# Optimization experiments

Measured on AMD Instinct MI355X. Metric: run time of the kernel, lower is better.

Reference implementation:

```python
import jax, jax.numpy as jnp
import numpy as np

L, B, S, D, H, FF, V = 4, 2, 1024, 768, 12, 3072, 50257
HD = D // H  # 64
EPS = 1e-5


def _ln(x, w, b):
    m = jnp.mean(x, axis=-1, keepdims=True)
    v = jnp.mean(jnp.square(x - m), axis=-1, keepdims=True)
    return (x - m) * jax.lax.rsqrt(v + EPS) * w + b


def setup_inputs() -> dict:
    key = jax.random.key(0)
    ks = jax.random.split(key, 8)
    std = 0.02
    inp = {
        'input_ids': jax.random.randint(ks[0], (B, S), 0, V),
        'tok_emb': jax.random.normal(ks[1], (V, D), jnp.float32) * std,
        'pos_emb': jax.random.normal(ks[2], (S, D), jnp.float32) * std,
        'ln1_w': jnp.ones((L, D), jnp.float32),
        'ln1_b': jnp.zeros((L, D), jnp.float32),
        'qkv_w': jax.random.normal(ks[3], (L, 3 * D, D), jnp.float32) * std,
        'qkv_b': jnp.zeros((L, 3 * D), jnp.float32),
        'out_w': jax.random.normal(ks[4], (L, D, D), jnp.float32) * std,
        'out_b': jnp.zeros((L, D), jnp.float32),
        'ln2_w': jnp.ones((L, D), jnp.float32),
        'ln2_b': jnp.zeros((L, D), jnp.float32),
        'fc1_w': jax.random.normal(ks[5], (L, FF, D), jnp.float32) * std,
        'fc1_b': jnp.zeros((L, FF), jnp.float32),
        'fc2_w': jax.random.normal(ks[6], (L, D, FF), jnp.float32) * std,
        'fc2_b': jnp.zeros((L, D), jnp.float32),
        'lnf_w': jnp.ones((D,), jnp.float32),
        'lnf_b': jnp.zeros((D,), jnp.float32),
    }
    return inp


def _gpt_forward(input_ids, tok_emb, pos_emb, ln1_w, ln1_b, qkv_w, qkv_b,
                 out_w, out_b, ln2_w, ln2_b, fc1_w, fc1_b, fc2_w, fc2_b,
                 lnf_w, lnf_b):
    x = tok_emb[input_ids] + pos_emb[None, :S, :]  # [B,S,D]
    causal = jnp.tril(jnp.ones((S, S), bool))  # [S,S]
    scale = 1.0 / np.sqrt(HD)
    for l in range(L):
        # --- attention ---
        h = _ln(x, ln1_w[l], ln1_b[l])
        qkv = h @ qkv_w[l].T + qkv_b[l]  # [B,S,3D]
        qkv = qkv.reshape(B, S, 3, H, HD).transpose(2, 0, 3, 1, 4)
        q, k, v = qkv[0], qkv[1], qkv[2]  # [B,H,S,HD]
        scores = jnp.einsum('bhqd,bhkd->bhqk', q, k) * scale
        scores = jnp.where(causal, scores, -jnp.inf)
        w = jax.nn.softmax(scores, axis=-1)
        a = jnp.einsum('bhqk,bhkd->bhqd', w, v)  # [B,H,S,HD]
        a = a.transpose(0, 2, 1, 3).reshape(B, S, D)
        x = x + a @ out_w[l].T + out_b[l]
        # --- ffn ---
        h = _ln(x, ln2_w[l], ln2_b[l])
        h = jax.nn.gelu(h @ fc1_w[l].T + fc1_b[l], approximate=False)
        x = x + h @ fc2_w[l].T + fc2_b[l]
    x = _ln(x, lnf_w, lnf_b)
    logits = x @ tok_emb.T  # tied lm_head, no bias
    return logits


def reference(input_ids, tok_emb, pos_emb, ln1_w, ln1_b, qkv_w, qkv_b,
              out_w, out_b, ln2_w, ln2_b, fc1_w, fc1_b, fc2_w, fc2_b,
              lnf_w, lnf_b):
    return _gpt_forward(input_ids, tok_emb, pos_emb, ln1_w, ln1_b, qkv_w,
                        qkv_b, out_w, out_b, ln2_w, ln2_b, fc1_w, fc1_b,
                        fc2_w, fc2_b, lnf_w, lnf_b)
```

## Files before the change

### kernel.cpp

```cpp
#include <hip/hip_runtime.h>
#include <cstdint>
#include <cstddef>

#define D_MODEL 768
#define NHEAD   12
#define SEQ     1024
#define NTOK    2048
#define FFDIM   3072
#define NLAYER  4
#define VOCAB   50257
#define QKVD    2304

typedef float f32x4 __attribute__((ext_vector_type(4)));
typedef __bf16 bf16x8 __attribute__((ext_vector_type(8)));

__device__ __forceinline__ unsigned short f2bf(float f) {
  unsigned int u = __float_as_uint(f);
  return (unsigned short)((u + 0x7FFFu + ((u >> 16) & 1u)) >> 16);
}

__global__ __launch_bounds__(256) void k_cvt(const float* __restrict__ in,
                                             unsigned short* __restrict__ out, int n8) {
  int i = blockIdx.x * 256 + threadIdx.x;
  if (i >= n8) return;
  const float4* p = (const float4*)in;
  float4 a = p[2 * i], b = p[2 * i + 1];
  union { unsigned short u[8]; uint4 v; } r;
  r.u[0] = f2bf(a.x); r.u[1] = f2bf(a.y); r.u[2] = f2bf(a.z); r.u[3] = f2bf(a.w);
  r.u[4] = f2bf(b.x); r.u[5] = f2bf(b.y); r.u[6] = f2bf(b.z); r.u[7] = f2bf(b.w);
  ((uint4*)out)[i] = r.v;
}

__global__ __launch_bounds__(256) void k_embed(const int* __restrict__ ids,
                                               const float* __restrict__ tok,
                                               const float* __restrict__ pos,
                                               float* __restrict__ x) {
  int gid = blockIdx.x * 256 + threadIdx.x;
  int t = gid / 192, f = gid - t * 192;
  int id = ids[t];
  float4 a = ((const float4*)tok)[(size_t)id * 192 + f];
  float4 b = ((const float4*)pos)[(size_t)(t & (SEQ - 1)) * 192 + f];
  float4 o; o.x = a.x + b.x; o.y = a.y + b.y; o.z = a.z + b.z; o.w = a.w + b.w;
  ((float4*)x)[gid] = o;
}

__global__ __launch_bounds__(256) void k_ln(const float* __restrict__ x,
                                            const float* __restrict__ w,
                                            const float* __restrict__ b,
                                            unsigned short* __restrict__ out) {
  __shared__ float red[256];
  int row = blockIdx.x, tid = threadIdx.x;
  const float* xr = x + (size_t)row * D_MODEL;
  float v0 = xr[tid], v1 = xr[tid + 256], v2 = xr[tid + 512];
  red[tid] = v0 + v1 + v2;
  __syncthreads();
  for (int o = 128; o > 0; o >>= 1) { if (tid < o) red[tid] += red[tid + o]; __syncthreads(); }
  float mean = red[0] * (1.0f / 768.0f);
  __syncthreads();
  float d0 = v0 - mean, d1 = v1 - mean, d2 = v2 - mean;
  red[tid] = d0 * d0 + d1 * d1 + d2 * d2;
  __syncthreads();
  for (int o = 128; o > 0; o >>= 1) { if (tid < o) red[tid] += red[tid + o]; __syncthreads(); }
  float rstd = rsqrtf(red[0] * (1.0f / 768.0f) + 1e-5f);
  unsigned short* orow = out + (size_t)row * D_MODEL;
  orow[tid]       = f2bf(d0 * rstd * w[tid]       + b[tid]);
  orow[tid + 256] = f2bf(d1 * rstd * w[tid + 256] + b[tid + 256]);
  orow[tid + 512] = f2bf(d2 * rstd * w[tid + 512] + b[tid + 512]);
}

__global__ __launch_bounds__(256) void k_vt(const unsigned short* __restrict__ qkv,
                                            unsigned short* __restrict__ vt) {
  __shared__ unsigned short t[64][80];
  int bid = blockIdx.x;
  int st = bid & 15, h = (bid >> 4) % NHEAD, b = bid / (16 * NHEAD);
  int tid = threadIdx.x;
  int r = tid >> 2, cq = (tid & 3) * 16;
  const unsigned short* src =
      qkv + (size_t)(b * SEQ + st * 64 + r) * QKVD + 2 * D_MODEL + h * 64 + cq;
  *(uint4*)&t[r][cq] = *(const uint4*)src;
  *(uint4*)&t[r][cq + 8] = *(const uint4*)(src + 8);
  __syncthreads();
  int d = r, j0 = cq;
  unsigned short* dst = vt + ((size_t)(b * D_MODEL) + h * 64 + d) * SEQ + st * 64 + j0;
  union { unsigned short u[8]; uint4 v; } o0, o1;
  #pragma unroll
  for (int jj = 0; jj < 8; ++jj) o0.u[jj] = t[j0 + jj][d];
  #pragma unroll
  for (int jj = 0; jj < 8; ++jj) o1.u[jj] = t[j0 + 8 + jj][d];
  *(uint4*)dst = o0.v;
  *(uint4*)(dst + 8) = o1.v;
}

__global__ __launch_bounds__(64) void k_attn(const unsigned short* __restrict__ qkv,
                                             const unsigned short* __restrict__ vt,
                                             unsigned short* __restrict__ attO) {
  int bid = blockIdx.x;
  int qt = (SEQ / 16 - 1) - (bid & 63);
  int h = (bid >> 6) % NHEAD;
  int b = bid / (64 * NHEAD);
  int lane = threadIdx.x;
  int fr = lane & 15, fq = lane >> 4;
  int qb = qt * 16;

  size_t rowQ = (size_t)(b * SEQ + qb + fr) * QKVD + h * 64;
  bf16x8 bq0 = *(const bf16x8*)(qkv + rowQ + fq * 8);
  bf16x8 bq1 = *(const bf16x8*)(qkv + rowQ + 32 + fq * 8);

  float m = -1e30f, ll = 0.0f;
  f32x4 o[4] = {};
  int nkt = (qt >> 1) + 1;
  size_t kvrow0 = (size_t)(b * SEQ) * QKVD;
  const unsigned short* vbase0 = vt + ((size_t)(b * D_MODEL) + h * 64 + fr) * SEQ;

  for (int kt = 0; kt < nkt; ++kt) {
    int kvb = kt * 32;
    bool diag = (kt == nkt - 1);
    float p[2][4];
    float tm = -1e30f;
    #pragma unroll
    for (int t = 0; t < 2; ++t) {
      size_t rowK = kvrow0 + (size_t)(kvb + t * 16 + fr) * QKVD + D_MODEL + h * 64;
      bf16x8 ak0 = *(const bf16x8*)(qkv + rowK + fq * 8);
      bf16x8 ak1 = *(const bf16x8*)(qkv + rowK + 32 + fq * 8);
      f32x4 st = {};
      st = __builtin_amdgcn_mfma_f32_16x16x32_bf16(ak0, bq0, st, 0, 0, 0);
      st = __builtin_amdgcn_mfma_f32_16x16x32_bf16(ak1, bq1, st, 0, 0, 0);
      #pragma unroll
      for (int j = 0; j < 4; ++j) {
        float s = st[j] * 0.125f;
        if (diag && (kvb + t * 16 + fq * 4 + j > qb + fr)) s = -1e30f;
        p[t][j] = s;
        tm = fmaxf(tm, s);
      }
    }
    tm = fmaxf(tm, __shfl_xor(tm, 16));
    tm = fmaxf(tm, __shfl_xor(tm, 32));
    float mnew = fmaxf(m, tm);
    float corr = __expf(m - mnew);
    float psum = 0.0f;
    #pragma unroll
    for (int t = 0; t < 2; ++t)
      #pragma unroll
      for (int j = 0; j < 4; ++j) { float e = __expf(p[t][j] - mnew); p[t][j] = e; psum += e; }
    psum += __shfl_xor(psum, 16);
    psum += __shfl_xor(psum, 32);
    ll = ll * corr + psum;
    m = mnew;
    #pragma unroll
    for (int dg = 0; dg < 4; ++dg) {
      o[dg][0] *= corr; o[dg][1] *= corr; o[dg][2] *= corr; o[dg][3] *= corr;
    }
    unsigned int lo0 = (unsigned)f2bf(p[0][0]) | ((unsigned)f2bf(p[0][1]) << 16);
    unsigned int hi0 = (unsigned)f2bf(p[0][2]) | ((unsigned)f2bf(p[0][3]) << 16);
    unsigned int lo1 = (unsigned)f2bf(p[1][0]) | ((unsigned)f2bf(p[1][1]) << 16);
    unsigned int hi1 = (unsigned)f2bf(p[1][2]) | ((unsigned)f2bf(p[1][3]) << 16);
    int sA = fr + 16 * ((fq & 1) * 2);
    int sB = sA + 16;
    unsigned int w0a = __shfl(lo0, sA), w0b = __shfl(lo1, sA);
    unsigned int w1a = __shfl(hi0, sA), w1b = __shfl(hi1, sA);
    unsigned int w2a = __shfl(lo0, sB), w2b = __shfl(lo1, sB);
    unsigned int w3a = __shfl(hi0, sB), w3b = __shfl(hi1, sB);
    bool t1 = (fq >> 1) != 0;
    uint4 pw;
    pw.x = t1 ? w0b : w0a;
    pw.y = t1 ? w1b : w1a;
    pw.z = t1 ? w2b : w2a;
    pw.w = t1 ? w3b : w3a;
    bf16x8 pb = __builtin_bit_cast(bf16x8, pw);
    const unsigned short* vp = vbase0 + kvb + fq * 8;
    #pragma unroll
    for (int dg = 0; dg < 4; ++dg) {
      bf16x8 va = *(const bf16x8*)(vp + (size_t)dg * 16 * SEQ);
      o[dg] = __builtin_amdgcn_mfma_f32_16x16x32_bf16(va, pb, o[dg], 0, 0, 0);
    }
  }
  float inv = 1.0f / ll;
  size_t obase = (size_t)(b * SEQ + qb + fr) * D_MODEL + h * 64;
  #pragma unroll
  for (int dg = 0; dg < 4; ++dg)
    #pragma unroll
    for (int j = 0; j < 4; ++j)
      attO[obase + dg * 16 + fq * 4 + j] = f2bf(o[dg][j] * inv);
}

template<int HAS_BIAS, int DO_GELU, int HAS_RES, int OUT_BF16>
__global__ __launch_bounds__(256) void k_gemm(const unsigned short* __restrict__ A,
                                              const unsigned short* __restrict__ W,
                                              const float* __restrict__ bias,
                                              const float* __restrict__ res,
                                              void* __restrict__ Cout,
                                              int N, int K) {
  __shared__ __align__(1024) unsigned short As[128 * 64];
  __shared__ __align__(1024) unsigned short Ws[128 * 64];
  int tid = threadIdx.x, lane = tid & 63, wv = tid >> 6;
  int fr = lane & 15, fq = lane >> 4;
  int wm = wv >> 1, wn = wv & 1;

  int cpx = gridDim.x >> 3;
  int id = (blockIdx.x & 7) * cpx + (blockIdx.x >> 3);
  int bm = (id & 15) * 128;
  int bn = (id >> 4) * 128;

  const unsigned short* pA[4];
  const unsigned short* pW[4];
  unsigned short* ldsA[4];
  unsigned short* ldsW[4];
  #pragma unroll
  for (int i = 0; i < 4; ++i) {
    int c = wv * 4 + i;
    int r = c * 8 + (lane >> 3);
    int up = (lane & 7) ^ (r & 7);
    pA[i] = A + (size_t)(bm + r) * K + up * 8;
    int wr = bn + r; if (wr > N - 1) wr = N - 1;
    pW[i] = W + (size_t)wr * K + up * 8;
    ldsA[i] = &As[c * 512];
    ldsW[i] = &Ws[c * 512];
  }

  const unsigned short* aB = As + (wm * 64 + fr) * 64;
  const unsigned short* wB = Ws + (wn * 64 + fr) * 64;
  int sz = fr & 7;
  int u0 = (fq ^ sz) * 8;
  int u1 = ((4 + fq) ^ sz) * 8;

  f32x4 acc[4][4] = {};

  for (int k0 = 0; k0 < K; k0 += 64) {
    #pragma unroll
    for (int i = 0; i < 4; ++i) {
      __builtin_amdgcn_global_load_lds(
          (const __attribute__((address_space(1))) unsigned int*)(pA[i] + k0),
          (__attribute__((address_space(3))) unsigned int*)ldsA[i], 16, 0, 0);
      __builtin_amdgcn_global_load_lds(
          (const __attribute__((address_space(1))) unsigned int*)(pW[i] + k0),
          (__attribute__((address_space(3))) unsigned int*)ldsW[i], 16, 0, 0);
    }
    __syncthreads();

    bf16x8 af[4][2], bf[4][2];
    #pragma unroll
    for (int mm = 0; mm < 4; ++mm) {
      af[mm][0] = *(const bf16x8*)(aB + mm * 1024 + u0);
      af[mm][1] = *(const bf16x8*)(aB + mm * 1024 + u1);
    }
    #pragma unroll
    for (int nn = 0; nn < 4; ++nn) {
      bf[nn][0] = *(const bf16x8*)(wB + nn * 1024 + u0);
      bf[nn][1] = *(const bf16x8*)(wB + nn * 1024 + u1);
    }
    #pragma unroll
    for (int mm = 0; mm < 4; ++mm)
      #pragma unroll
      for (int nn = 0; nn < 4; ++nn) {
        acc[mm][nn] = __builtin_amdgcn_mfma_f32_16x16x32_bf16(af[mm][0], bf[nn][0], acc[mm][nn], 0, 0, 0);
        acc[mm][nn] = __builtin_amdgcn_mfma_f32_16x16x32_bf16(af[mm][1], bf[nn][1], acc[mm][nn], 0, 0, 0);
      }
    __syncthreads();
  }

  #pragma unroll
  for (int nn = 0; nn < 4; ++nn) {
    int col = bn + wn * 64 + nn * 16 + fr;
    if (col >= N) continue;
    float bv = HAS_BIAS ? bias[col] : 0.0f;
    #pragma unroll
    for (int mm = 0; mm < 4; ++mm) {
      #pragma unroll
      for (int j = 0; j < 4; ++j) {
        int row = bm + wm * 64 + mm * 16 + fq * 4 + j;
        size_t idx = (size_t)row * N + col;
        float v = acc[mm][nn][j] + bv;
        if (DO_GELU) v = 0.5f * v * (1.0f + erff(v * 0.70710678118f));
        if (HAS_RES) v += res[idx];
        if (OUT_BF16) ((unsigned short*)Cout)[idx] = f2bf(v);
        else          ((float*)Cout)[idx] = v;
      }
    }
  }
}

extern "C" void kernel_launch(void* const* d_in, const int* in_sizes, int n_in,
                              void* d_out, int out_size, void* d_ws, size_t ws_size,
                              hipStream_t stream) {
  const int*   ids    = (const int*)d_in[0];
  const float* tok    = (const float*)d_in[1];
  const float* pos    = (const float*)d_in[2];
  const float* ln1_w  = (const float*)d_in[3];
  const float* ln1_b  = (const float*)d_in[4];
  const float* qkv_w  = (const float*)d_in[5];
  const float* qkv_b  = (const float*)d_in[6];
  const float* out_w  = (const float*)d_in[7];
  const float* out_b  = (const float*)d_in[8];
  const float* ln2_w  = (const float*)d_in[9];
  const float* ln2_b  = (const float*)d_in[10];
  const float* fc1_w  = (const float*)d_in[11];
  const float* fc1_b  = (const float*)d_in[12];
  const float* fc2_w  = (const float*)d_in[13];
  const float* fc2_b  = (const float*)d_in[14];
  const float* lnf_w  = (const float*)d_in[15];
  const float* lnf_b  = (const float*)d_in[16];

  char* ws = (char*)d_ws;
  float*          x    = (float*)(ws);
  unsigned short* qkvb = (unsigned short*)(ws + 6291456);
  unsigned short* h    = (unsigned short*)(ws + 15728640);
  unsigned short* attO = (unsigned short*)(ws + 18874368);
  unsigned short* gbuf = (unsigned short*)(ws + 22020096);
  unsigned short* wq   = (unsigned short*)(ws + 34603008);
  unsigned short* wo   = (unsigned short*)(ws + 48758784);
  unsigned short* w1   = (unsigned short*)(ws + 53477376);
  unsigned short* w2   = (unsigned short*)(ws + 72351744);
  unsigned short* wtok = (unsigned short*)(ws + 91226112);
  float* logits = (float*)d_out;

  {
    int n8;
    n8 = NLAYER * QKVD * D_MODEL / 8;
    k_cvt<<<(n8 + 255) / 256, 256, 0, stream>>>(qkv_w, wq, n8);
    n8 = NLAYER * D_MODEL * D_MODEL / 8;
    k_cvt<<<(n8 + 255) / 256, 256, 0, stream>>>(out_w, wo, n8);
    n8 = NLAYER * FFDIM * D_MODEL / 8;
    k_cvt<<<(n8 + 255) / 256, 256, 0, stream>>>(fc1_w, w1, n8);
    k_cvt<<<(n8 + 255) / 256, 256, 0, stream>>>(fc2_w, w2, n8);
    n8 = VOCAB * D_MODEL / 8;
    k_cvt<<<(n8 + 255) / 256, 256, 0, stream>>>(tok, wtok, n8);
  }

  k_embed<<<NTOK * 192 / 256, 256, 0, stream>>>(ids, tok, pos, x);

  for (int l = 0; l < NLAYER; ++l) {
    k_ln<<<NTOK, 256, 0, stream>>>(x, ln1_w + l * D_MODEL, ln1_b + l * D_MODEL, h);
    k_gemm<1, 0, 0, 1><<<16 * (QKVD / 128), 256, 0, stream>>>(
        h, wq + (size_t)l * QKVD * D_MODEL, qkv_b + l * QKVD, nullptr, qkvb, QKVD, D_MODEL);
    k_vt<<<2 * NHEAD * 16, 256, 0, stream>>>(qkvb, h);
    k_attn<<<2 * NHEAD * (SEQ / 16), 64, 0, stream>>>(qkvb, h, attO);
    k_gemm<1, 0, 1, 0><<<16 * (D_MODEL / 128), 256, 0, stream>>>(
        attO, wo + (size_t)l * D_MODEL * D_MODEL, out_b + l * D_MODEL, x, x, D_MODEL, D_MODEL);
    k_ln<<<NTOK, 256, 0, stream>>>(x, ln2_w + l * D_MODEL, ln2_b + l * D_MODEL, h);
    k_gemm<1, 1, 0, 1><<<16 * (FFDIM / 128), 256, 0, stream>>>(
        h, w1 + (size_t)l * FFDIM * D_MODEL, fc1_b + l * FFDIM, nullptr, gbuf, FFDIM, D_MODEL);
    k_gemm<1, 0, 1, 0><<<16 * (D_MODEL / 128), 256, 0, stream>>>(
        gbuf, w2 + (size_t)l * D_MODEL * FFDIM, fc2_b + l * D_MODEL, x, x, D_MODEL, FFDIM);
  }

  k_ln<<<NTOK, 256, 0, stream>>>(x, lnf_w, lnf_b, h);
  k_gemm<0, 0, 0, 0><<<16 * ((VOCAB + 127) / 128), 256, 0, stream>>>(
      h, wtok, nullptr, nullptr, logits, VOCAB, D_MODEL);
}
```

Measured before the change: 1.202 ms.

## Merge weight conversions into one launch and load GEMM A tiles directly to registers

The five separate fp32-to-bf16 weight conversion launches become a single kernel that picks its source and destination by offset range, which removes launch overhead and the tail gaps between launches. In the GEMM, the A operand is no longer staged through LDS. Each lane reads its bf16x8 fragments straight from global memory, which halves LDS use and traffic. The cost is uncoalesced row-strided global loads for A that may rely on cache hits, and the loads are no longer shared across the waves that reuse the same rows.

```diff
diff --git a/kernel.cpp b/kernel.cpp
--- a/kernel.cpp
+++ b/kernel.cpp
@@ -19,16 +19,23 @@
   return (unsigned short)((u + 0x7FFFu + ((u >> 16) & 1u)) >> 16);
 }
 
-__global__ __launch_bounds__(256) void k_cvt(const float* __restrict__ in,
-                                             unsigned short* __restrict__ out, int n8) {
-  int i = blockIdx.x * 256 + threadIdx.x;
-  if (i >= n8) return;
-  const float4* p = (const float4*)in;
-  float4 a = p[2 * i], b = p[2 * i + 1];
+__global__ __launch_bounds__(256) void k_cvt5(const float* __restrict__ s0, unsigned short* __restrict__ d0, int n0,
+                                              const float* __restrict__ s1, unsigned short* __restrict__ d1, int n1,
+                                              const float* __restrict__ s2, unsigned short* __restrict__ d2, int n2,
+                                              const float* __restrict__ s3, unsigned short* __restrict__ d3, int n3,
+                                              const float* __restrict__ s4, unsigned short* __restrict__ d4, int n4) {
+  int off = blockIdx.x * 256 + threadIdx.x;
+  const float* s; unsigned short* d;
+  if (off < n0) { s = s0; d = d0; }
+  else { off -= n0; if (off < n1) { s = s1; d = d1; }
+  else { off -= n1; if (off < n2) { s = s2; d = d2; }
+  else { off -= n2; if (off < n3) { s = s3; d = d3; }
+  else { off -= n3; if (off >= n4) return; s = s4; d = d4; } } } }
+  float4 a = ((const float4*)s)[2 * off], b = ((const float4*)s)[2 * off + 1];
   union { unsigned short u[8]; uint4 v; } r;
   r.u[0] = f2bf(a.x); r.u[1] = f2bf(a.y); r.u[2] = f2bf(a.z); r.u[3] = f2bf(a.w);
   r.u[4] = f2bf(b.x); r.u[5] = f2bf(b.y); r.u[6] = f2bf(b.z); r.u[7] = f2bf(b.w);
-  ((uint4*)out)[i] = r.v;
+  ((uint4*)d)[off] = r.v;
 }
 
 __global__ __launch_bounds__(256) void k_embed(const int* __restrict__ ids,
@@ -190,7 +197,6 @@
                                               const float* __restrict__ res,
                                               void* __restrict__ Cout,
                                               int N, int K) {
-  __shared__ __align__(1024) unsigned short As[128 * 64];
   __shared__ __align__(1024) unsigned short Ws[128 * 64];
   int tid = threadIdx.x, lane = tid & 63, wv = tid >> 6;
   int fr = lane & 15, fq = lane >> 4;
@@ -201,23 +207,20 @@
   int bm = (id & 15) * 128;
   int bn = (id >> 4) * 128;
 
-  const unsigned short* pA[4];
   const unsigned short* pW[4];
-  unsigned short* ldsA[4];
   unsigned short* ldsW[4];
   #pragma unroll
   for (int i = 0; i < 4; ++i) {
     int c = wv * 4 + i;
     int r = c * 8 + (lane >> 3);
     int up = (lane & 7) ^ (r & 7);
-    pA[i] = A + (size_t)(bm + r) * K + up * 8;
     int wr = bn + r; if (wr > N - 1) wr = N - 1;
     pW[i] = W + (size_t)wr * K + up * 8;
-    ldsA[i] = &As[c * 512];
     ldsW[i] = &Ws[c * 512];
   }
 
-  const unsigned short* aB = As + (wm * 64 + fr) * 64;
+  const unsigned short* aP = A + (size_t)(bm + wm * 64 + fr) * K + fq * 8;
+
   const unsigned short* wB = Ws + (wn * 64 + fr) * 64;
   int sz = fr & 7;
   int u0 = (fq ^ sz) * 8;
@@ -226,23 +229,21 @@
   f32x4 acc[4][4] = {};
 
   for (int k0 = 0; k0 < K; k0 += 64) {
+    bf16x8 af[4][2];
+    #pragma unroll
+    for (int mm = 0; mm < 4; ++mm) {
+      af[mm][0] = *(const bf16x8*)(aP + (size_t)mm * 16 * K + k0);
+      af[mm][1] = *(const bf16x8*)(aP + (size_t)mm * 16 * K + k0 + 32);
+    }
     #pragma unroll
     for (int i = 0; i < 4; ++i) {
-      __builtin_amdgcn_global_load_lds(
-          (const __attribute__((address_space(1))) unsigned int*)(pA[i] + k0),
-          (__attribute__((address_space(3))) unsigned int*)ldsA[i], 16, 0, 0);
       __builtin_amdgcn_global_load_lds(
           (const __attribute__((address_space(1))) unsigned int*)(pW[i] + k0),
           (__attribute__((address_space(3))) unsigned int*)ldsW[i], 16, 0, 0);
     }
     __syncthreads();
 
-    bf16x8 af[4][2], bf[4][2];
-    #pragma unroll
-    for (int mm = 0; mm < 4; ++mm) {
-      af[mm][0] = *(const bf16x8*)(aB + mm * 1024 + u0);
-      af[mm][1] = *(const bf16x8*)(aB + mm * 1024 + u1);
-    }
+    bf16x8 bf[4][2];
     #pragma unroll
     for (int nn = 0; nn < 4; ++nn) {
       bf[nn][0] = *(const bf16x8*)(wB + nn * 1024 + u0);
@@ -314,16 +315,14 @@
   float* logits = (float*)d_out;
 
   {
-    int n8;
-    n8 = NLAYER * QKVD * D_MODEL / 8;
-    k_cvt<<<(n8 + 255) / 256, 256, 0, stream>>>(qkv_w, wq, n8);
-    n8 = NLAYER * D_MODEL * D_MODEL / 8;
-    k_cvt<<<(n8 + 255) / 256, 256, 0, stream>>>(out_w, wo, n8);
-    n8 = NLAYER * FFDIM * D_MODEL / 8;
-    k_cvt<<<(n8 + 255) / 256, 256, 0, stream>>>(fc1_w, w1, n8);
-    k_cvt<<<(n8 + 255) / 256, 256, 0, stream>>>(fc2_w, w2, n8);
-    n8 = VOCAB * D_MODEL / 8;
-    k_cvt<<<(n8 + 255) / 256, 256, 0, stream>>>(tok, wtok, n8);
+    int n0 = NLAYER * QKVD * D_MODEL / 8;
+    int n1 = NLAYER * D_MODEL * D_MODEL / 8;
+    int n2 = NLAYER * FFDIM * D_MODEL / 8;
+    int n3 = n2;
+    int n4 = VOCAB * D_MODEL / 8;
+    int tot = n0 + n1 + n2 + n3 + n4;
+    k_cvt5<<<(tot + 255) / 256, 256, 0, stream>>>(
+        qkv_w, wq, n0, out_w, wo, n1, fc1_w, w1, n2, fc2_w, w2, n3, tok, wtok, n4);
   }
 
   k_embed<<<NTOK * 192 / 256, 256, 0, stream>>>(ids, tok, pos, x);
```

Result: slower. 1.454 ms (+20.9%).
